# Performance work log

Hardware: AMD Instinct MI355X
Metric: run time of the kernel (lower is better)

The kernel has to match this reference:

```python
import jax, jax.numpy as jnp
import numpy as np

EPS = 1e-5
NUM_HEADS = 16
NUM_KV_HEADS = 4
NUM_EXPERTS = 8
TOP_K = 2


def _layernorm(x, w, b):
    mu = jnp.mean(x, axis=-1, keepdims=True)
    var = jnp.mean((x - mu) ** 2, axis=-1, keepdims=True)
    return (x - mu) * jax.lax.rsqrt(var + EPS) * w + b


def setup_inputs() -> dict:
    key = jax.random.key(0)
    ks = jax.random.split(key, 8)
    S, B, H = 1024, 4, 1024
    F = 2048
    hd = H // NUM_HEADS
    qkv_out = (NUM_HEADS + 2 * NUM_KV_HEADS) * hd  # 1536
    w_scale = 0.02
    return {
        "hidden_states": jax.random.normal(ks[0], (S, B, H), jnp.float32),
        "ln1_weight": jnp.ones((H,), jnp.float32),
        "ln1_bias": jnp.zeros((H,), jnp.float32),
        "ln2_weight": jnp.ones((H,), jnp.float32),
        "ln2_bias": jnp.zeros((H,), jnp.float32),
        "qkv_weight": jax.random.normal(ks[1], (qkv_out, H), jnp.float32) * w_scale,
        "proj_weight": jax.random.normal(ks[2], (H, H), jnp.float32) * w_scale,
        "router_weight": jax.random.normal(ks[3], (NUM_EXPERTS, H), jnp.float32) * w_scale,
        "moe_w1": jax.random.normal(ks[4], (NUM_EXPERTS, H, F), jnp.float32) * w_scale,
        "moe_w2": jax.random.normal(ks[5], (NUM_EXPERTS, F, H), jnp.float32) * w_scale,
    }


def reference(hidden_states, ln1_weight, ln1_bias, ln2_weight, ln2_bias,
              qkv_weight, proj_weight, router_weight, moe_w1, moe_w2):
    S, B, H = hidden_states.shape
    hd = H // NUM_HEADS
    rep = NUM_HEADS // NUM_KV_HEADS
    scale = 1.0 / hd ** 0.5

    # LN1 -> fused QKV projection
    ln1_out = _layernorm(hidden_states, ln1_weight, ln1_bias)
    qkv = jnp.einsum('sbh,oh->sbo', ln1_out, qkv_weight)
    q = qkv[..., :NUM_HEADS * hd].reshape(S, B, NUM_HEADS, hd)
    k = qkv[..., NUM_HEADS * hd:(NUM_HEADS + NUM_KV_HEADS) * hd].reshape(S, B, NUM_KV_HEADS, hd)
    v = qkv[..., (NUM_HEADS + NUM_KV_HEADS) * hd:].reshape(S, B, NUM_KV_HEADS, hd)

    # GQA: repeat KV heads to match query heads
    k = jnp.repeat(k, rep, axis=2)
    v = jnp.repeat(v, rep, axis=2)

    # causal scaled dot-product attention
    scores = jnp.einsum('sbhd,tbhd->bhst', q, k) * scale  # [B,h,S,S]
    causal = jnp.tril(jnp.ones((S, S), bool))
    scores = jnp.where(causal, scores, jnp.finfo(scores.dtype).min)
    probs = jax.nn.softmax(scores, axis=-1)
    attn = jnp.einsum('bhst,tbhd->sbhd', probs, v).reshape(S, B, H)

    proj_out = jnp.einsum('sbh,oh->sbo', attn, proj_weight)
    hidden_after_attn = hidden_states + proj_out

    # LN2 -> MoE
    ln2_out = _layernorm(hidden_after_attn, ln2_weight, ln2_bias)
    x = ln2_out.reshape(-1, H)  # [T,H]

    logits = jnp.einsum('th,eh->te', x, router_weight)
    gate = jax.nn.softmax(logits, axis=-1)
    top_probs, top_idx = jax.lax.top_k(gate, TOP_K)  # [T,K]

    # dense all-expert FFN (reference for grouped expert GEMMs)
    h_mid = jax.nn.gelu(jnp.einsum('th,ehf->etf', x, moe_w1))  # [E,T,F]
    expert_out = jnp.einsum('etf,efh->eth', h_mid, moe_w2)     # [E,T,H]

    # combine: weight[e,t] = sum_k top_probs[t,k] * (top_idx[t,k]==e)
    e_ids = jnp.arange(NUM_EXPERTS)[:, None, None]
    weights = jnp.sum(jnp.where(top_idx[None] == e_ids, top_probs[None], 0.0), axis=-1)  # [E,T]
    moe_out = jnp.einsum('eth,et->th', expert_out, weights).reshape(S, B, H)

    return hidden_after_attn + moe_out
```

## Files before the change

### kernel.cpp

```cpp
#include <hip/hip_runtime.h>
#include <stdint.h>

typedef unsigned short u16;
typedef float f32x4 __attribute__((ext_vector_type(4)));
typedef __bf16 bf16x8 __attribute__((ext_vector_type(8)));
typedef u16 u16x8 __attribute__((ext_vector_type(8)));

#define NHEADS 16
#define NKV 4
#define HD 64
#define HDIM 1024
#define FDIM 2048
#define SLEN 1024
#define BATCH 4
#define TTOK 4096
#define NEXP 8
#define QKVO 1536
#define K3 3072
#define NREP 32

__device__ __forceinline__ u16 f2bf(float f) {
  union { float f; uint32_t u; } c; c.f = f;
  uint32_t u = c.u;
  return (u16)((u + 0x7FFFu + ((u >> 16) & 1u)) >> 16);
}
__device__ __forceinline__ float bf2f(u16 h) {
  union { uint32_t u; float f; } c; c.u = ((uint32_t)h) << 16; return c.f;
}
__device__ __forceinline__ void split2(float v, u16& h, u16& l) {
  h = f2bf(v);
  l = f2bf(v - bf2f(h));
}

__device__ __forceinline__ f32x4 mfma16(bf16x8 a, bf16x8 b, f32x4 c) {
  return __builtin_amdgcn_mfma_f32_16x16x32_bf16(a, b, c, 0, 0, 0);
}

__device__ __forceinline__ bf16x8 lds_frag(const u16* base) {
  u16x8 v = *(const u16x8*)base;
  return __builtin_bit_cast(bf16x8, v);
}

__device__ __forceinline__ void gload_lds16(const void* g, void* l) {
  __builtin_amdgcn_global_load_lds((const __attribute__((address_space(1))) void*)g,
                                   (__attribute__((address_space(3))) void*)l, 16, 0, 0);
}

__global__ __launch_bounds__(256)
void cvt_w3_kernel(const float* __restrict__ in, u16* __restrict__ out, int n4) {
  int i = blockIdx.x * blockDim.x + threadIdx.x;
  if (i >= n4) return;
  float4 v = ((const float4*)in)[i];
  int row = i >> 8;
  int c = (i & 255) * 4;
  ushort4 h, l;
  split2(v.x, h.x, l.x); split2(v.y, h.y, l.y);
  split2(v.z, h.z, l.z); split2(v.w, h.w, l.w);
  u16* orow = out + (size_t)row * K3 + c;
  *(ushort4*)(orow) = h;
  *(ushort4*)(orow + 1024) = h;
  *(ushort4*)(orow + 2048) = l;
}

__global__ __launch_bounds__(256)
void transpose_cvt_kernel(const float* __restrict__ in, u16* __restrict__ out, int R, int C) {
  __shared__ float tile[32][33];
  size_t eoff = (size_t)blockIdx.z * (size_t)R * (size_t)C;
  in += eoff; out += eoff;
  int c0 = blockIdx.x * 32, r0 = blockIdx.y * 32;
  int tx = threadIdx.x, ty = threadIdx.y;
#pragma unroll
  for (int i = 0; i < 4; i++)
    tile[ty + i * 8][tx] = in[(size_t)(r0 + ty + i * 8) * C + c0 + tx];
  __syncthreads();
#pragma unroll
  for (int i = 0; i < 4; i++)
    out[(size_t)(c0 + ty + i * 8) * R + r0 + tx] = f2bf(tile[tx][ty + i * 8]);
}

__global__ __launch_bounds__(256)
void ln_kernel(const float* __restrict__ x, const float* __restrict__ w,
               const float* __restrict__ bias, u16* __restrict__ o3,
               u16* __restrict__ obf, float* __restrict__ of32) {
  int t = blockIdx.x, tid = threadIdx.x;
  int wid = tid >> 6, lane = tid & 63;
  float4 v = ((const float4*)(x + (size_t)t * HDIM))[tid];
  float s = v.x + v.y + v.z + v.w;
  float q = v.x * v.x + v.y * v.y + v.z * v.z + v.w * v.w;
#pragma unroll
  for (int mm = 32; mm >= 1; mm >>= 1) {
    s += __shfl_xor(s, mm);
    q += __shfl_xor(q, mm);
  }
  __shared__ float ss[4], qq[4];
  if (lane == 0) { ss[wid] = s; qq[wid] = q; }
  __syncthreads();
  s = ss[0] + ss[1] + ss[2] + ss[3];
  q = qq[0] + qq[1] + qq[2] + qq[3];
  float mu = s * (1.0f / HDIM);
  float var = q * (1.0f / HDIM) - mu * mu;
  float inv = rsqrtf(var + 1e-5f);
  float4 wv = ((const float4*)w)[tid];
  float4 bv = ((const float4*)bias)[tid];
  float y0 = (v.x - mu) * inv * wv.x + bv.x;
  float y1 = (v.y - mu) * inv * wv.y + bv.y;
  float y2 = (v.z - mu) * inv * wv.z + bv.z;
  float y3 = (v.w - mu) * inv * wv.w + bv.w;
  ushort4 h, l;
  split2(y0, h.x, l.x); split2(y1, h.y, l.y);
  split2(y2, h.z, l.z); split2(y3, h.w, l.w);
  if (o3) {
    u16* orow = o3 + (size_t)t * K3 + tid * 4;
    *(ushort4*)(orow) = h;
    *(ushort4*)(orow + 1024) = l;
    *(ushort4*)(orow + 2048) = h;
  }
  if (obf) ((ushort4*)(obf + (size_t)t * HDIM))[tid] = h;
  if (of32) {
    float4 yo; yo.x = y0; yo.y = y1; yo.z = y2; yo.w = y3;
    ((float4*)(of32 + (size_t)t * HDIM))[tid] = yo;
  }
}

template<int MODE>
__global__ __launch_bounds__(256)
void gemm_bt(const u16* __restrict__ A0, const u16* __restrict__ B0,
             int N, int K, int M,
             const float* __restrict__ resid, float* __restrict__ outf,
             u16* __restrict__ o0, u16* __restrict__ o1, u16* __restrict__ o2,
             u16* __restrict__ o3, u16* __restrict__ o4, u16* __restrict__ o5,
             const int* __restrict__ offs, const int* __restrict__ rowsIdx,
             const float* __restrict__ wts) {
  int tid = threadIdx.x;
  int wid = tid >> 6, lane = tid & 63;
  int l15 = lane & 15, l4 = lane >> 4;
  int bn = blockIdx.x, bm = blockIdx.y, e = blockIdx.z;

  int Me = M, rowBase = 0;
  const u16* A = A0;
  const u16* B = B0;
  if constexpr (MODE == 2 || MODE == 3) {
    int oa = offs[e], ob = offs[e + 1];
    Me = ob - oa; rowBase = oa;
    B = B0 + (size_t)e * (size_t)N * (size_t)K;
    if constexpr (MODE == 3) A = A0 + (size_t)oa * (size_t)K;
  }
  if (bm * 128 >= Me) return;

  __shared__ u16 lsA[2][128 * 64];
  __shared__ u16 lsB[2][128 * 64];

  int slot = tid & 7;
  const u16* aPtr[4];
  const u16* bPtr[4];
#pragma unroll
  for (int i = 0; i < 4; i++) {
    int r = i * 32 + (tid >> 3);
    int sl = slot ^ (r & 7);
    int rg = bm * 128 + r;
    if constexpr (MODE == 2) {
      int rc = rg < Me ? rg : (Me - 1);
      rg = rowsIdx[rowBase + rc];
    } else if constexpr (MODE == 3) {
      rg = rg < Me ? rg : (Me - 1);
    }
    aPtr[i] = A + (size_t)rg * K + sl * 8;
    int ng = bn * 128 + r;
    bPtr[i] = B + (size_t)ng * K + sl * 8;
  }

  int wm = (wid >> 1) * 64, wn = (wid & 1) * 64;
  f32x4 zero4 = {0.f, 0.f, 0.f, 0.f};
  f32x4 acc[4][4];
#pragma unroll
  for (int mi = 0; mi < 4; mi++)
#pragma unroll
    for (int ni = 0; ni < 4; ni++) acc[mi][ni] = zero4;

  int aoff[4][2], boff[4][2];
#pragma unroll
  for (int mi = 0; mi < 4; mi++) {
    int row = wm + mi * 16 + l15;
#pragma unroll
    for (int kk = 0; kk < 2; kk++) {
      int cs = kk * 4 + l4;
      aoff[mi][kk] = row * 64 + ((cs ^ (row & 7)) << 3);
    }
  }
#pragma unroll
  for (int ni = 0; ni < 4; ni++) {
    int row = wn + ni * 16 + l15;
#pragma unroll
    for (int kk = 0; kk < 2; kk++) {
      int cs = kk * 4 + l4;
      boff[ni][kk] = row * 64 + ((cs ^ (row & 7)) << 3);
    }
  }

  int nk = K >> 6;
#pragma unroll
  for (int i = 0; i < 4; i++) {
    gload_lds16(aPtr[i], &lsA[0][(i * 256 + wid * 64) * 8]);
    gload_lds16(bPtr[i], &lsB[0][(i * 256 + wid * 64) * 8]);
  }
  __syncthreads();

  int buf = 0;
  for (int kt = 0; kt < nk; ++kt) {
    if (kt + 1 < nk) {
      int k0 = (kt + 1) << 6;
#pragma unroll
      for (int i = 0; i < 4; i++) {
        gload_lds16(aPtr[i] + k0, &lsA[buf ^ 1][(i * 256 + wid * 64) * 8]);
        gload_lds16(bPtr[i] + k0, &lsB[buf ^ 1][(i * 256 + wid * 64) * 8]);
      }
    }
#pragma unroll
    for (int kk = 0; kk < 2; kk++) {
      bf16x8 af[4], bfr[4];
#pragma unroll
      for (int mi = 0; mi < 4; mi++) af[mi] = lds_frag(&lsA[buf][aoff[mi][kk]]);
#pragma unroll
      for (int ni = 0; ni < 4; ni++) bfr[ni] = lds_frag(&lsB[buf][boff[ni][kk]]);
#pragma unroll
      for (int mi = 0; mi < 4; mi++)
#pragma unroll
        for (int ni = 0; ni < 4; ni++)
          acc[mi][ni] = mfma16(af[mi], bfr[ni], acc[mi][ni]);
    }
    __syncthreads();
    buf ^= 1;
  }

#pragma unroll
  for (int mi = 0; mi < 4; mi++) {
#pragma unroll
    for (int r = 0; r < 4; r++) {
      int m = bm * 128 + wm + mi * 16 + l4 * 4 + r;
      if (m >= Me) continue;
#pragma unroll
      for (int ni = 0; ni < 4; ni++) {
        int n = bn * 128 + wn + ni * 16 + l15;
        float v = acc[mi][ni][r];
        if constexpr (MODE == 0) {
          u16 hh, ll; split2(v, hh, ll);
          int sq = m >> 2, bb = m & 3;
          int d = n & 63;
          if (n < 1024) {
            int hd = n >> 6;
            size_t o = ((size_t)(bb * NHEADS + hd) * SLEN + sq) * HD + d;
            o0[o] = hh; o1[o] = ll;
          } else if (n < 1280) {
            int hd = (n - 1024) >> 6;
            size_t o = ((size_t)(bb * NKV + hd) * SLEN + sq) * HD + d;
            o2[o] = hh; o3[o] = ll;
          } else {
            int hd = (n - 1280) >> 6;
            size_t o = ((size_t)(bb * NKV + hd) * SLEN + sq) * HD + d;
            o4[o] = hh; o5[o] = ll;
          }
        } else if constexpr (MODE == 1) {
          size_t idx = (size_t)m * HDIM + n;
          outf[idx] = v + resid[idx];
        } else if constexpr (MODE == 2) {
          float g = 0.5f * v * (1.0f + tanhf(0.7978845608f * (v + 0.044715f * v * v * v)));
          o0[(size_t)(rowBase + m) * FDIM + n] = f2bf(g);
        } else {
          outf[(size_t)(rowBase + m) * HDIM + n] = v * wts[rowBase + m];
        }
      }
    }
  }
}

__global__ __launch_bounds__(256)
void attn_kernel(const u16* __restrict__ Qh_, const u16* __restrict__ Ql_,
                 const u16* __restrict__ Kh_, const u16* __restrict__ Kl_,
                 const u16* __restrict__ Vh_, const u16* __restrict__ Vl_,
                 u16* __restrict__ A3) {
  int bh = blockIdx.x;
  int qt = blockIdx.y;
  int b = bh >> 4, h = bh & 15, kh = h >> 2;
  int tid = threadIdx.x, wid = tid >> 6, lane = tid & 63;
  int l15 = lane & 15, l4 = lane >> 4;
  int slot = tid & 7;

  size_t qoff = ((size_t)(b * NHEADS + h) * SLEN) * HD;
  size_t koff = ((size_t)(b * NKV + kh) * SLEN) * HD;
  const u16* Qh = Qh_ + qoff;
  const u16* Ql = Ql_ + qoff;
  const u16* Kh = Kh_ + koff;
  const u16* Kl = Kl_ + koff;
  const u16* Vh = Vh_ + koff;
  const u16* Vl = Vl_ + koff;

  __shared__ u16 KtH[2][4096], KtL[2][4096];
  __shared__ u16 VtH[4096], VtL[4096];
  __shared__ u16 PtH[4][1024], PtL[4][1024];

  int qrow = qt * 64 + wid * 16 + l15;
  bf16x8 qfh[2], qfl[2];
#pragma unroll
  for (int kk = 0; kk < 2; kk++) {
    u16x8 vh = *(const u16x8*)(Qh + (size_t)qrow * HD + kk * 32 + l4 * 8);
    u16x8 vl = *(const u16x8*)(Ql + (size_t)qrow * HD + kk * 32 + l4 * 8);
    qfh[kk] = __builtin_bit_cast(bf16x8, vh);
    qfl[kk] = __builtin_bit_cast(bf16x8, vl);
  }

  int kr0 = tid >> 3;
  int kr1 = 32 + (tid >> 3);
  int sl0 = slot ^ (kr0 & 7);
  int sl1 = slot ^ (kr1 & 7);
  int kdst0 = (0 * 256 + wid * 64) * 8;
  int kdst1 = (1 * 256 + wid * 64) * 8;

#define STAGE_K(kt_, bf_)                                                     \
  {                                                                           \
    size_t s0 = (size_t)((kt_)*64 + kr0) * HD + sl0 * 8;                      \
    size_t s1 = (size_t)((kt_)*64 + kr1) * HD + sl1 * 8;                      \
    gload_lds16(Kh + s0, &KtH[bf_][kdst0]);                                   \
    gload_lds16(Kl + s0, &KtL[bf_][kdst0]);                                   \
    gload_lds16(Kh + s1, &KtH[bf_][kdst1]);                                   \
    gload_lds16(Kl + s1, &KtL[bf_][kdst1]);                                   \
  }

#define LOAD_V(kt_, vh_, vl_)                                                 \
  {                                                                           \
    _Pragma("unroll") for (int i = 0; i < 2; i++) {                           \
      int kv = i * 32 + (tid >> 3);                                           \
      (vh_)[i] = *(const uint4*)(Vh + (size_t)((kt_)*64 + kv) * HD + slot * 8);\
      (vl_)[i] = *(const uint4*)(Vl + (size_t)((kt_)*64 + kv) * HD + slot * 8);\
    }                                                                         \
  }

#define SCATTER_V(vh_, vl_)                                                   \
  {                                                                           \
    _Pragma("unroll") for (int i = 0; i < 2; i++) {                           \
      int kv = i * 32 + (tid >> 3);                                           \
      const u16* ph = (const u16*)&(vh_)[i];                                  \
      const u16* pl = (const u16*)&(vl_)[i];                                  \
      _Pragma("unroll") for (int j = 0; j < 8; j++) {                         \
        int d = slot * 8 + j;                                                 \
        int g = ((kv >> 3) ^ (d & 7) ^ (d >> 3)) & 7;                         \
        int addr = d * 64 + (g << 3) + (kv & 7);                              \
        VtH[addr] = ph[j];                                                    \
        VtL[addr] = pl[j];                                                    \
      }                                                                       \
    }                                                                         \
  }

  uint4 vH[2], vL[2];
  STAGE_K(0, 0);
  LOAD_V(0, vH, vL);
  SCATTER_V(vH, vL);
  __syncthreads();

  f32x4 zero4 = {0.f, 0.f, 0.f, 0.f};
  f32x4 oacc[4];
#pragma unroll
  for (int nf = 0; nf < 4; nf++) oacc[nf] = zero4;
  float mrun[4], lrun[4];
#pragma unroll
  for (int r = 0; r < 4; r++) { mrun[r] = -1e30f; lrun[r] = 0.f; }

  int buf = 0;
  for (int kt = 0; kt <= qt; ++kt) {
    int kv0 = kt * 64;
    if (kt < qt) {
      STAGE_K(kt + 1, buf ^ 1);
      LOAD_V(kt + 1, vH, vL);
    }

    f32x4 sacc[4];
#pragma unroll
    for (int nf = 0; nf < 4; nf++) sacc[nf] = zero4;
#pragma unroll
    for (int kk = 0; kk < 2; kk++) {
#pragma unroll
      for (int nf = 0; nf < 4; nf++) {
        int krow = nf * 16 + l15;
        int ka = krow * 64 + (((kk * 4 + l4) ^ (krow & 7)) << 3);
        bf16x8 kfh = lds_frag(&KtH[buf][ka]);
        bf16x8 kfl = lds_frag(&KtL[buf][ka]);
        sacc[nf] = mfma16(qfh[kk], kfh, sacc[nf]);
        sacc[nf] = mfma16(qfh[kk], kfl, sacc[nf]);
        sacc[nf] = mfma16(qfl[kk], kfh, sacc[nf]);
      }
    }

    bool diag = (kt == qt);
    float tm[4];
#pragma unroll
    for (int r = 0; r < 4; r++) tm[r] = -1e30f;
#pragma unroll
    for (int nf = 0; nf < 4; nf++) {
#pragma unroll
      for (int r = 0; r < 4; r++) {
        float s = sacc[nf][r] * 0.125f;
        if (diag) {
          int qg = qt * 64 + wid * 16 + l4 * 4 + r;
          int kg = kv0 + nf * 16 + l15;
          if (kg > qg) s = -1e30f;
        }
        sacc[nf][r] = s;
        tm[r] = fmaxf(tm[r], s);
      }
    }
#pragma unroll
    for (int mm = 1; mm < 16; mm <<= 1) {
#pragma unroll
      for (int r = 0; r < 4; r++) tm[r] = fmaxf(tm[r], __shfl_xor(tm[r], mm));
    }
    float ts[4];
#pragma unroll
    for (int r = 0; r < 4; r++) {
      float mn = fmaxf(mrun[r], tm[r]);
      float al = __expf(mrun[r] - mn);
      mrun[r] = mn;
      lrun[r] *= al;
#pragma unroll
      for (int nf = 0; nf < 4; nf++) oacc[nf][r] *= al;
      ts[r] = 0.f;
    }
#pragma unroll
    for (int nf = 0; nf < 4; nf++) {
#pragma unroll
      for (int r = 0; r < 4; r++) {
        float p = __expf(sacc[nf][r] - mrun[r]);
        sacc[nf][r] = p;
        ts[r] += p;
      }
    }
#pragma unroll
    for (int mm = 1; mm < 16; mm <<= 1) {
#pragma unroll
      for (int r = 0; r < 4; r++) ts[r] += __shfl_xor(ts[r], mm);
    }
#pragma unroll
    for (int r = 0; r < 4; r++) lrun[r] += ts[r];

#pragma unroll
    for (int nf = 0; nf < 4; nf++) {
#pragma unroll
      for (int r = 0; r < 4; r++) {
        int qrl = l4 * 4 + r;
        int kv = nf * 16 + l15;
        int g = ((kv >> 3) ^ (qrl & 7) ^ (qrl >> 3)) & 7;
        int addr = qrl * 64 + (g << 3) + (kv & 7);
        u16 hh, ll;
        split2(sacc[nf][r], hh, ll);
        PtH[wid][addr] = hh;
        PtL[wid][addr] = ll;
      }
    }
#pragma unroll
    for (int s2 = 0; s2 < 2; s2++) {
      int cs = s2 * 4 + l4;
      int pa = l15 * 64 + ((((cs ^ (l15 & 7) ^ (l15 >> 3))) & 7) << 3);
      bf16x8 pfh = lds_frag(&PtH[wid][pa]);
      bf16x8 pfl = lds_frag(&PtL[wid][pa]);
#pragma unroll
      for (int nf = 0; nf < 4; nf++) {
        int d = nf * 16 + l15;
        int va = d * 64 + ((((cs ^ (d & 7) ^ (d >> 3))) & 7) << 3);
        bf16x8 vfh = lds_frag(&VtH[va]);
        bf16x8 vfl = lds_frag(&VtL[va]);
        oacc[nf] = mfma16(pfh, vfh, oacc[nf]);
        oacc[nf] = mfma16(pfh, vfl, oacc[nf]);
        oacc[nf] = mfma16(pfl, vfh, oacc[nf]);
      }
    }

    __syncthreads();
    if (kt < qt) {
      SCATTER_V(vH, vL);
    }
    __syncthreads();
    buf ^= 1;
  }

#pragma unroll
  for (int r = 0; r < 4; r++) {
    float invl = 1.0f / lrun[r];
    int qg = qt * 64 + wid * 16 + l4 * 4 + r;
    size_t tb = ((size_t)qg * BATCH + b) * K3 + h * HD;
#pragma unroll
    for (int nf = 0; nf < 4; nf++) {
      u16 hh, ll;
      split2(oacc[nf][r] * invl, hh, ll);
      size_t o = tb + nf * 16 + l15;
      A3[o] = hh;
      A3[o + 1024] = ll;
      A3[o + 2048] = hh;
    }
  }
#undef STAGE_K
#undef LOAD_V
#undef SCATTER_V
}

__global__ __launch_bounds__(256)
void router_kernel(const float* __restrict__ x, const float* __restrict__ rw,
                   int* __restrict__ tidx, float* __restrict__ tp) {
  int t = blockIdx.x, tid = threadIdx.x;
  int wid = tid >> 6, lane = tid & 63;
  float4 xv = ((const float4*)(x + (size_t)t * HDIM))[tid];
  __shared__ float part[8][4];
  __shared__ float lg[8];
#pragma unroll
  for (int e = 0; e < 8; e++) {
    float4 wv = ((const float4*)(rw + (size_t)e * HDIM))[tid];
    float d = xv.x * wv.x + xv.y * wv.y + xv.z * wv.z + xv.w * wv.w;
#pragma unroll
    for (int mm = 32; mm >= 1; mm >>= 1) d += __shfl_xor(d, mm);
    if (lane == 0) part[e][wid] = d;
  }
  __syncthreads();
  if (tid < 8) lg[tid] = part[tid][0] + part[tid][1] + part[tid][2] + part[tid][3];
  __syncthreads();
  if (tid == 0) {
    float mx = lg[0];
#pragma unroll
    for (int e = 1; e < 8; e++) mx = fmaxf(mx, lg[e]);
    float g[8]; float se = 0.f;
#pragma unroll
    for (int e = 0; e < 8; e++) { g[e] = __expf(lg[e] - mx); se += g[e]; }
    float inv = 1.0f / se;
#pragma unroll
    for (int e = 0; e < 8; e++) g[e] *= inv;
    int i0 = 0; float v0 = g[0];
#pragma unroll
    for (int e = 1; e < 8; e++) if (g[e] > v0) { v0 = g[e]; i0 = e; }
    int i1 = -1; float v1 = -1.f;
#pragma unroll
    for (int e = 0; e < 8; e++) if (e != i0 && g[e] > v1) { v1 = g[e]; i1 = e; }
    tidx[t * 2] = i0; tidx[t * 2 + 1] = i1;
    tp[t * 2] = v0; tp[t * 2 + 1] = v1;
  }
}

__global__ __launch_bounds__(256)
void hist_offsets_kernel(const int* __restrict__ tidx, int* __restrict__ offs,
                         int* __restrict__ repBase, int* __restrict__ curRep) {
  __shared__ int hist[NEXP * NREP];
  __shared__ int eoffs[NEXP + 1];
  int tid = threadIdx.x;
  hist[tid] = 0;
  __syncthreads();
  for (int i = tid; i < TTOK; i += 256) {
    int rep = i & (NREP - 1);
    atomicAdd(&hist[tidx[2 * i] * NREP + rep], 1);
    atomicAdd(&hist[tidx[2 * i + 1] * NREP + rep], 1);
  }
  __syncthreads();
  if (tid == 0) {
    int a = 0;
    for (int e = 0; e < NEXP; e++) {
      eoffs[e] = a;
      for (int r = 0; r < NREP; r++) a += hist[e * NREP + r];
    }
    eoffs[NEXP] = a;
  }
  __syncthreads();
  if (tid < NEXP) {
    int a = eoffs[tid];
    for (int r = 0; r < NREP; r++) {
      repBase[tid * NREP + r] = a;
      a += hist[tid * NREP + r];
    }
  }
  if (tid < NEXP + 1) offs[tid] = eoffs[tid];
  curRep[tid] = 0;
}

__global__ __launch_bounds__(256)
void assign_kernel(const int* __restrict__ tidx, const float* __restrict__ tp,
                   const int* __restrict__ repBase, int* __restrict__ curRep,
                   int* __restrict__ rowsIdx, float* __restrict__ wvals,
                   int* __restrict__ inv) {
  int t = blockIdx.x * blockDim.x + threadIdx.x;
  if (t >= TTOK) return;
  int rep = t & (NREP - 1);
#pragma unroll
  for (int k = 0; k < 2; k++) {
    int e = tidx[t * 2 + k];
    int s = atomicAdd(&curRep[e * NREP + rep], 1);
    int pos = repBase[e * NREP + rep] + s;
    rowsIdx[pos] = t;
    wvals[pos] = tp[t * 2 + k];
    inv[t * 2 + k] = pos;
  }
}

__global__ __launch_bounds__(256)
void combine_kernel(float* __restrict__ out, const float* __restrict__ eo,
                    const int* __restrict__ inv) {
  int t = blockIdx.x, c = threadIdx.x;
  int r0 = inv[t * 2], r1 = inv[t * 2 + 1];
  float4* o = (float4*)(out + (size_t)t * HDIM);
  const float4* e0 = (const float4*)(eo + (size_t)r0 * HDIM);
  const float4* e1 = (const float4*)(eo + (size_t)r1 * HDIM);
  float4 v = o[c];
  float4 a = e0[c];
  float4 bb = e1[c];
  v.x += a.x + bb.x; v.y += a.y + bb.y; v.z += a.z + bb.z; v.w += a.w + bb.w;
  o[c] = v;
}

extern "C" void kernel_launch(void* const* d_in, const int* in_sizes, int n_in,
                              void* d_out, int out_size, void* d_ws, size_t ws_size,
                              hipStream_t stream) {
  (void)in_sizes; (void)n_in; (void)out_size; (void)ws_size;
  const float* hs    = (const float*)d_in[0];
  const float* ln1w  = (const float*)d_in[1];
  const float* ln1b  = (const float*)d_in[2];
  const float* ln2w  = (const float*)d_in[3];
  const float* ln2b  = (const float*)d_in[4];
  const float* wqkv  = (const float*)d_in[5];
  const float* wproj = (const float*)d_in[6];
  const float* wrout = (const float*)d_in[7];
  const float* w1    = (const float*)d_in[8];
  const float* w2    = (const float*)d_in[9];
  float* out = (float*)d_out;

  char* base = (char*)d_ws;
  size_t off = 0;
  auto alloc = [&](size_t n) { void* r = base + off; off += (n + 255) & ~(size_t)255; return r; };

  const size_t SZ_W1T   = (size_t)NEXP * FDIM * HDIM * 2;
  const size_t SZ_W2T   = (size_t)NEXP * HDIM * FDIM * 2;
  const size_t SZ_WP3   = (size_t)HDIM * K3 * 2;
  const size_t SZ_LN13  = (size_t)TTOK * K3 * 2;
  const size_t SZ_WQ3   = (size_t)QKVO * K3 * 2;
  const size_t SZ_HMID  = (size_t)TTOK * 2 * FDIM * 2;
  const size_t SZ_Q     = (size_t)BATCH * NHEADS * SLEN * HD * 2;
  const size_t SZ_KV    = (size_t)BATCH * NKV * SLEN * HD * 2;
  const size_t SZ_A3    = (size_t)TTOK * K3 * 2;
  const size_t SZ_EO    = (size_t)TTOK * 2 * HDIM * 4;

  u16* w1t     = (u16*)alloc(SZ_W1T);
  u16* w2t     = (u16*)alloc(SZ_W2T);
  u16* wproj3  = (u16*)alloc(SZ_WP3);

  size_t r1sz = SZ_LN13 + SZ_WQ3;
  if (SZ_HMID > r1sz) r1sz = SZ_HMID;
  char* r1 = (char*)alloc(r1sz);
  u16* ln1_3 = (u16*)r1;
  u16* wqkv3 = (u16*)(r1 + SZ_LN13);
  u16* hmid  = (u16*)r1;

  size_t r2sz = 2 * SZ_Q + 4 * SZ_KV + SZ_A3;
  if (SZ_EO > r2sz) r2sz = SZ_EO;
  char* r2 = (char*)alloc(r2sz);
  u16* Qbh = (u16*)r2;
  u16* Qbl = (u16*)(r2 + SZ_Q);
  u16* Kbh = (u16*)(r2 + 2 * SZ_Q);
  u16* Kbl = (u16*)(r2 + 2 * SZ_Q + SZ_KV);
  u16* Vbh = (u16*)(r2 + 2 * SZ_Q + 2 * SZ_KV);
  u16* Vbl = (u16*)(r2 + 2 * SZ_Q + 3 * SZ_KV);
  u16* attn3 = (u16*)(r2 + 2 * SZ_Q + 4 * SZ_KV);
  float* eo = (float*)r2;

  u16* ln2o    = (u16*)alloc((size_t)TTOK * HDIM * 2);
  float* ln2f  = (float*)alloc((size_t)TTOK * HDIM * 4);
  int* tidx    = (int*)alloc(TTOK * 2 * 4);
  float* tp    = (float*)alloc(TTOK * 2 * 4);
  int* rowsIdx = (int*)alloc(TTOK * 2 * 4);
  float* wvals = (float*)alloc(TTOK * 2 * 4);
  int* invm    = (int*)alloc(TTOK * 2 * 4);
  int* offs    = (int*)alloc((NEXP + 1) * 4);
  int* repBase = (int*)alloc(NEXP * NREP * 4);
  int* curRep  = (int*)alloc(NEXP * NREP * 4);

  cvt_w3_kernel<<<(QKVO * HDIM / 4 + 255) / 256, 256, 0, stream>>>(wqkv, wqkv3, QKVO * HDIM / 4);
  cvt_w3_kernel<<<(HDIM * HDIM / 4 + 255) / 256, 256, 0, stream>>>(wproj, wproj3, HDIM * HDIM / 4);
  dim3 tb(32, 8);
  transpose_cvt_kernel<<<dim3(FDIM / 32, HDIM / 32, NEXP), tb, 0, stream>>>(w1, w1t, HDIM, FDIM);
  transpose_cvt_kernel<<<dim3(HDIM / 32, FDIM / 32, NEXP), tb, 0, stream>>>(w2, w2t, FDIM, HDIM);

  ln_kernel<<<TTOK, 256, 0, stream>>>(hs, ln1w, ln1b, ln1_3, nullptr, nullptr);

  gemm_bt<0><<<dim3(QKVO / 128, TTOK / 128), 256, 0, stream>>>(
      ln1_3, wqkv3, QKVO, K3, TTOK, nullptr, nullptr,
      Qbh, Qbl, Kbh, Kbl, Vbh, Vbl, nullptr, nullptr, nullptr);

  attn_kernel<<<dim3(BATCH * NHEADS, SLEN / 64), 256, 0, stream>>>(
      Qbh, Qbl, Kbh, Kbl, Vbh, Vbl, attn3);

  gemm_bt<1><<<dim3(HDIM / 128, TTOK / 128), 256, 0, stream>>>(
      attn3, wproj3, HDIM, K3, TTOK, hs, out,
      nullptr, nullptr, nullptr, nullptr, nullptr, nullptr, nullptr, nullptr, nullptr);

  ln_kernel<<<TTOK, 256, 0, stream>>>(out, ln2w, ln2b, nullptr, ln2o, ln2f);

  router_kernel<<<TTOK, 256, 0, stream>>>(ln2f, wrout, tidx, tp);
  hist_offsets_kernel<<<1, 256, 0, stream>>>(tidx, offs, repBase, curRep);
  assign_kernel<<<TTOK / 256, 256, 0, stream>>>(tidx, tp, repBase, curRep, rowsIdx, wvals, invm);

  gemm_bt<2><<<dim3(FDIM / 128, TTOK / 128, NEXP), 256, 0, stream>>>(
      ln2o, w1t, FDIM, HDIM, 0, nullptr, nullptr,
      hmid, nullptr, nullptr, nullptr, nullptr, nullptr, offs, rowsIdx, nullptr);

  gemm_bt<3><<<dim3(HDIM / 128, TTOK / 128, NEXP), 256, 0, stream>>>(
      hmid, w2t, HDIM, FDIM, 0, nullptr, eo,
      nullptr, nullptr, nullptr, nullptr, nullptr, nullptr, offs, nullptr, wvals);

  combine_kernel<<<TTOK, 256, 0, stream>>>(out, eo, invm);
}
```

Baseline: 484.5 us.

## Shrink split-bf16 operands to 2K layout, add XCD remap and larger MoE tiles

```diff
diff --git a/kernel.cpp b/kernel.cpp
--- a/kernel.cpp
+++ b/kernel.cpp
@@ -16,7 +16,7 @@
 #define TTOK 4096
 #define NEXP 8
 #define QKVO 1536
-#define K3 3072
+#define K2 2048
 #define NREP 32
 
 __device__ __forceinline__ u16 f2bf(float f) {
@@ -47,7 +47,7 @@
 }
 
 __global__ __launch_bounds__(256)
-void cvt_w3_kernel(const float* __restrict__ in, u16* __restrict__ out, int n4) {
+void cvt_w2_kernel(const float* __restrict__ in, u16* __restrict__ out, int n4) {
   int i = blockIdx.x * blockDim.x + threadIdx.x;
   if (i >= n4) return;
   float4 v = ((const float4*)in)[i];
@@ -56,10 +56,9 @@
   ushort4 h, l;
   split2(v.x, h.x, l.x); split2(v.y, h.y, l.y);
   split2(v.z, h.z, l.z); split2(v.w, h.w, l.w);
-  u16* orow = out + (size_t)row * K3 + c;
+  u16* orow = out + (size_t)row * K2 + c;
   *(ushort4*)(orow) = h;
-  *(ushort4*)(orow + 1024) = h;
-  *(ushort4*)(orow + 2048) = l;
+  *(ushort4*)(orow + 1024) = l;
 }
 
 __global__ __launch_bounds__(256)
@@ -80,7 +79,7 @@
 
 __global__ __launch_bounds__(256)
 void ln_kernel(const float* __restrict__ x, const float* __restrict__ w,
-               const float* __restrict__ bias, u16* __restrict__ o3,
+               const float* __restrict__ bias, u16* __restrict__ o2,
                u16* __restrict__ obf, float* __restrict__ of32) {
   int t = blockIdx.x, tid = threadIdx.x;
   int wid = tid >> 6, lane = tid & 63;
@@ -109,11 +108,10 @@
   ushort4 h, l;
   split2(y0, h.x, l.x); split2(y1, h.y, l.y);
   split2(y2, h.z, l.z); split2(y3, h.w, l.w);
-  if (o3) {
-    u16* orow = o3 + (size_t)t * K3 + tid * 4;
+  if (o2) {
+    u16* orow = o2 + (size_t)t * K2 + tid * 4;
     *(ushort4*)(orow) = h;
     *(ushort4*)(orow + 1024) = l;
-    *(ushort4*)(orow + 2048) = h;
   }
   if (obf) ((ushort4*)(obf + (size_t)t * HDIM))[tid] = h;
   if (of32) {
@@ -122,19 +120,31 @@
   }
 }
 
-template<int MODE>
-__global__ __launch_bounds__(256)
+template<int MODE, int TB, int BM>
+__global__ __launch_bounds__(TB, 2)
 void gemm_bt(const u16* __restrict__ A0, const u16* __restrict__ B0,
-             int N, int K, int M,
+             int kstride, int nk, int M,
              const float* __restrict__ resid, float* __restrict__ outf,
              u16* __restrict__ o0, u16* __restrict__ o1, u16* __restrict__ o2,
              u16* __restrict__ o3, u16* __restrict__ o4, u16* __restrict__ o5,
              const int* __restrict__ offs, const int* __restrict__ rowsIdx,
              const float* __restrict__ wts) {
+  constexpr int BN = 128;
+  constexpr int IA = BM / (TB / 8);
+  constexpr int IB = BN / (TB / 8);
   int tid = threadIdx.x;
   int wid = tid >> 6, lane = tid & 63;
   int l15 = lane & 15, l4 = lane >> 4;
-  int bn = blockIdx.x, bm = blockIdx.y, e = blockIdx.z;
+  int slot = tid & 7;
+
+  int gx = gridDim.x;
+  int nwg = gx * gridDim.y;
+  int flat = blockIdx.y * gx + blockIdx.x;
+  int q8 = nwg >> 3, r8 = nwg & 7;
+  int xcd = flat & 7, idx = flat >> 3;
+  int nf = (xcd < r8 ? xcd * (q8 + 1) : r8 * (q8 + 1) + (xcd - r8) * q8) + idx;
+  int bn = nf % gx, bm = nf / gx;
+  int e = blockIdx.z;
 
   int Me = M, rowBase = 0;
   const u16* A = A0;
@@ -142,31 +152,34 @@
   if constexpr (MODE == 2 || MODE == 3) {
     int oa = offs[e], ob = offs[e + 1];
     Me = ob - oa; rowBase = oa;
-    B = B0 + (size_t)e * (size_t)N * (size_t)K;
-    if constexpr (MODE == 3) A = A0 + (size_t)oa * (size_t)K;
-  }
-  if (bm * 128 >= Me) return;
-
-  __shared__ u16 lsA[2][128 * 64];
-  __shared__ u16 lsB[2][128 * 64];
-
-  int slot = tid & 7;
-  const u16* aPtr[4];
-  const u16* bPtr[4];
-#pragma unroll
-  for (int i = 0; i < 4; i++) {
-    int r = i * 32 + (tid >> 3);
+    B = B0 + (size_t)e * (size_t)(MODE == 2 ? FDIM : HDIM) * (size_t)kstride;
+    if constexpr (MODE == 3) A = A0 + (size_t)oa * (size_t)kstride;
+  }
+  if (bm * BM >= Me) return;
+
+  __shared__ u16 lsA[2][BM * 64];
+  __shared__ u16 lsB[2][BN * 64];
+
+  const u16* aPtr[IA];
+  const u16* bPtr[IB];
+#pragma unroll
+  for (int i = 0; i < IA; i++) {
+    int r = (i * TB + tid) >> 3;
     int sl = slot ^ (r & 7);
-    int rg = bm * 128 + r;
+    int rg = bm * BM + r;
     if constexpr (MODE == 2) {
       int rc = rg < Me ? rg : (Me - 1);
       rg = rowsIdx[rowBase + rc];
     } else if constexpr (MODE == 3) {
       rg = rg < Me ? rg : (Me - 1);
     }
-    aPtr[i] = A + (size_t)rg * K + sl * 8;
-    int ng = bn * 128 + r;
-    bPtr[i] = B + (size_t)ng * K + sl * 8;
+    aPtr[i] = A + (size_t)rg * kstride + sl * 8;
+  }
+#pragma unroll
+  for (int i = 0; i < IB; i++) {
+    int r = (i * TB + tid) >> 3;
+    int sl = slot ^ (r & 7);
+    bPtr[i] = B + (size_t)(bn * BN + r) * kstride + sl * 8;
   }
 
   int wm = (wid >> 1) * 64, wn = (wid & 1) * 64;
@@ -197,23 +210,33 @@
     }
   }
 
-  int nk = K >> 6;
-#pragma unroll
-  for (int i = 0; i < 4; i++) {
-    gload_lds16(aPtr[i], &lsA[0][(i * 256 + wid * 64) * 8]);
-    gload_lds16(bPtr[i], &lsB[0][(i * 256 + wid * 64) * 8]);
-  }
+  auto ksched = [&](int kt, int& ak, int& bk) {
+    if constexpr (MODE <= 1) {
+      int ph = kt >> 4, kl = kt & 15;
+      ak = (ph == 1 ? 1024 : 0) + kl * 64;
+      bk = (ph == 2 ? 1024 : 0) + kl * 64;
+    } else {
+      ak = kt << 6;
+      bk = ak;
+    }
+  };
+
+  int ak, bk;
+  ksched(0, ak, bk);
+#pragma unroll
+  for (int i = 0; i < IA; i++) gload_lds16(aPtr[i] + ak, &lsA[0][(i * TB + wid * 64) * 8]);
+#pragma unroll
+  for (int i = 0; i < IB; i++) gload_lds16(bPtr[i] + bk, &lsB[0][(i * TB + wid * 64) * 8]);
   __syncthreads();
 
   int buf = 0;
   for (int kt = 0; kt < nk; ++kt) {
     if (kt + 1 < nk) {
-      int k0 = (kt + 1) << 6;
-#pragma unroll
-      for (int i = 0; i < 4; i++) {
-        gload_lds16(aPtr[i] + k0, &lsA[buf ^ 1][(i * 256 + wid * 64) * 8]);
-        gload_lds16(bPtr[i] + k0, &lsB[buf ^ 1][(i * 256 + wid * 64) * 8]);
-      }
+      ksched(kt + 1, ak, bk);
+#pragma unroll
+      for (int i = 0; i < IA; i++) gload_lds16(aPtr[i] + ak, &lsA[buf ^ 1][(i * TB + wid * 64) * 8]);
+#pragma unroll
+      for (int i = 0; i < IB; i++) gload_lds16(bPtr[i] + bk, &lsB[buf ^ 1][(i * TB + wid * 64) * 8]);
     }
 #pragma unroll
     for (int kk = 0; kk < 2; kk++) {
@@ -236,11 +259,11 @@
   for (int mi = 0; mi < 4; mi++) {
 #pragma unroll
     for (int r = 0; r < 4; r++) {
-      int m = bm * 128 + wm + mi * 16 + l4 * 4 + r;
+      int m = bm * BM + wm + mi * 16 + l4 * 4 + r;
       if (m >= Me) continue;
 #pragma unroll
       for (int ni = 0; ni < 4; ni++) {
-        int n = bn * 128 + wn + ni * 16 + l15;
+        int n = bn * BN + wn + ni * 16 + l15;
         float v = acc[mi][ni][r];
         if constexpr (MODE == 0) {
           u16 hh, ll; split2(v, hh, ll);
@@ -260,8 +283,8 @@
             o4[o] = hh; o5[o] = ll;
           }
         } else if constexpr (MODE == 1) {
-          size_t idx = (size_t)m * HDIM + n;
-          outf[idx] = v + resid[idx];
+          size_t iidx = (size_t)m * HDIM + n;
+          outf[iidx] = v + resid[iidx];
         } else if constexpr (MODE == 2) {
           float g = 0.5f * v * (1.0f + tanhf(0.7978845608f * (v + 0.044715f * v * v * v)));
           o0[(size_t)(rowBase + m) * FDIM + n] = f2bf(g);
@@ -277,7 +300,7 @@
 void attn_kernel(const u16* __restrict__ Qh_, const u16* __restrict__ Ql_,
                  const u16* __restrict__ Kh_, const u16* __restrict__ Kl_,
                  const u16* __restrict__ Vh_, const u16* __restrict__ Vl_,
-                 u16* __restrict__ A3) {
+                 u16* __restrict__ A2) {
   int bh = blockIdx.x;
   int qt = blockIdx.y;
   int b = bh >> 4, h = bh & 15, kh = h >> 2;
@@ -484,15 +507,14 @@
   for (int r = 0; r < 4; r++) {
     float invl = 1.0f / lrun[r];
     int qg = qt * 64 + wid * 16 + l4 * 4 + r;
-    size_t tb = ((size_t)qg * BATCH + b) * K3 + h * HD;
+    size_t tb = ((size_t)qg * BATCH + b) * K2 + h * HD;
 #pragma unroll
     for (int nf = 0; nf < 4; nf++) {
       u16 hh, ll;
       split2(oacc[nf][r] * invl, hh, ll);
       size_t o = tb + nf * 16 + l15;
-      A3[o] = hh;
-      A3[o + 1024] = ll;
-      A3[o + 2048] = hh;
+      A2[o] = hh;
+      A2[o + 1024] = ll;
     }
   }
 #undef STAGE_K
@@ -630,27 +652,27 @@
 
   const size_t SZ_W1T   = (size_t)NEXP * FDIM * HDIM * 2;
   const size_t SZ_W2T   = (size_t)NEXP * HDIM * FDIM * 2;
-  const size_t SZ_WP3   = (size_t)HDIM * K3 * 2;
-  const size_t SZ_LN13  = (size_t)TTOK * K3 * 2;
-  const size_t SZ_WQ3   = (size_t)QKVO * K3 * 2;
+  const size_t SZ_WP2   = (size_t)HDIM * K2 * 2;
+  const size_t SZ_LN12  = (size_t)TTOK * K2 * 2;
+  const size_t SZ_WQ2   = (size_t)QKVO * K2 * 2;
   const size_t SZ_HMID  = (size_t)TTOK * 2 * FDIM * 2;
   const size_t SZ_Q     = (size_t)BATCH * NHEADS * SLEN * HD * 2;
   const size_t SZ_KV    = (size_t)BATCH * NKV * SLEN * HD * 2;
-  const size_t SZ_A3    = (size_t)TTOK * K3 * 2;
+  const size_t SZ_A2    = (size_t)TTOK * K2 * 2;
   const size_t SZ_EO    = (size_t)TTOK * 2 * HDIM * 4;
 
   u16* w1t     = (u16*)alloc(SZ_W1T);
   u16* w2t     = (u16*)alloc(SZ_W2T);
-  u16* wproj3  = (u16*)alloc(SZ_WP3);
-
-  size_t r1sz = SZ_LN13 + SZ_WQ3;
+  u16* wproj2  = (u16*)alloc(SZ_WP2);
+
+  size_t r1sz = SZ_LN12 + SZ_WQ2;
   if (SZ_HMID > r1sz) r1sz = SZ_HMID;
   char* r1 = (char*)alloc(r1sz);
-  u16* ln1_3 = (u16*)r1;
-  u16* wqkv3 = (u16*)(r1 + SZ_LN13);
+  u16* ln1_2 = (u16*)r1;
+  u16* wqkv2 = (u16*)(r1 + SZ_LN12);
   u16* hmid  = (u16*)r1;
 
-  size_t r2sz = 2 * SZ_Q + 4 * SZ_KV + SZ_A3;
+  size_t r2sz = 2 * SZ_Q + 4 * SZ_KV + SZ_A2;
   if (SZ_EO > r2sz) r2sz = SZ_EO;
   char* r2 = (char*)alloc(r2sz);
   u16* Qbh = (u16*)r2;
@@ -659,7 +681,7 @@
   u16* Kbl = (u16*)(r2 + 2 * SZ_Q + SZ_KV);
   u16* Vbh = (u16*)(r2 + 2 * SZ_Q + 2 * SZ_KV);
   u16* Vbl = (u16*)(r2 + 2 * SZ_Q + 3 * SZ_KV);
-  u16* attn3 = (u16*)(r2 + 2 * SZ_Q + 4 * SZ_KV);
+  u16* attn2 = (u16*)(r2 + 2 * SZ_Q + 4 * SZ_KV);
   float* eo = (float*)r2;
 
   u16* ln2o    = (u16*)alloc((size_t)TTOK * HDIM * 2);
@@ -673,23 +695,23 @@
   int* repBase = (int*)alloc(NEXP * NREP * 4);
   int* curRep  = (int*)alloc(NEXP * NREP * 4);
 
-  cvt_w3_kernel<<<(QKVO * HDIM / 4 + 255) / 256, 256, 0, stream>>>(wqkv, wqkv3, QKVO * HDIM / 4);
-  cvt_w3_kernel<<<(HDIM * HDIM / 4 + 255) / 256, 256, 0, stream>>>(wproj, wproj3, HDIM * HDIM / 4);
+  cvt_w2_kernel<<<(QKVO * HDIM / 4 + 255) / 256, 256, 0, stream>>>(wqkv, wqkv2, QKVO * HDIM / 4);
+  cvt_w2_kernel<<<(HDIM * HDIM / 4 + 255) / 256, 256, 0, stream>>>(wproj, wproj2, HDIM * HDIM / 4);
   dim3 tb(32, 8);
   transpose_cvt_kernel<<<dim3(FDIM / 32, HDIM / 32, NEXP), tb, 0, stream>>>(w1, w1t, HDIM, FDIM);
   transpose_cvt_kernel<<<dim3(HDIM / 32, FDIM / 32, NEXP), tb, 0, stream>>>(w2, w2t, FDIM, HDIM);
 
-  ln_kernel<<<TTOK, 256, 0, stream>>>(hs, ln1w, ln1b, ln1_3, nullptr, nullptr);
-
-  gemm_bt<0><<<dim3(QKVO / 128, TTOK / 128), 256, 0, stream>>>(
-      ln1_3, wqkv3, QKVO, K3, TTOK, nullptr, nullptr,
+  ln_kernel<<<TTOK, 256, 0, stream>>>(hs, ln1w, ln1b, ln1_2, nullptr, nullptr);
+
+  gemm_bt<0, 256, 128><<<dim3(QKVO / 128, TTOK / 128), 256, 0, stream>>>(
+      ln1_2, wqkv2, K2, 48, TTOK, nullptr, nullptr,
       Qbh, Qbl, Kbh, Kbl, Vbh, Vbl, nullptr, nullptr, nullptr);
 
   attn_kernel<<<dim3(BATCH * NHEADS, SLEN / 64), 256, 0, stream>>>(
-      Qbh, Qbl, Kbh, Kbl, Vbh, Vbl, attn3);
-
-  gemm_bt<1><<<dim3(HDIM / 128, TTOK / 128), 256, 0, stream>>>(
-      attn3, wproj3, HDIM, K3, TTOK, hs, out,
+      Qbh, Qbl, Kbh, Kbl, Vbh, Vbl, attn2);
+
+  gemm_bt<1, 256, 128><<<dim3(HDIM / 128, TTOK / 128), 256, 0, stream>>>(
+      attn2, wproj2, K2, 48, TTOK, hs, out,
       nullptr, nullptr, nullptr, nullptr, nullptr, nullptr, nullptr, nullptr, nullptr);
 
   ln_kernel<<<TTOK, 256, 0, stream>>>(out, ln2w, ln2b, nullptr, ln2o, ln2f);
@@ -698,12 +720,12 @@
   hist_offsets_kernel<<<1, 256, 0, stream>>>(tidx, offs, repBase, curRep);
   assign_kernel<<<TTOK / 256, 256, 0, stream>>>(tidx, tp, repBase, curRep, rowsIdx, wvals, invm);
 
-  gemm_bt<2><<<dim3(FDIM / 128, TTOK / 128, NEXP), 256, 0, stream>>>(
-      ln2o, w1t, FDIM, HDIM, 0, nullptr, nullptr,
+  gemm_bt<2, 512, 256><<<dim3(FDIM / 128, 16, NEXP), 512, 0, stream>>>(
+      ln2o, w1t, HDIM, 16, 0, nullptr, nullptr,
       hmid, nullptr, nullptr, nullptr, nullptr, nullptr, offs, rowsIdx, nullptr);
 
-  gemm_bt<3><<<dim3(HDIM / 128, TTOK / 128, NEXP), 256, 0, stream>>>(
-      hmid, w2t, HDIM, FDIM, 0, nullptr, eo,
+  gemm_bt<3, 512, 256><<<dim3(HDIM / 128, 16, NEXP), 512, 0, stream>>>(
+      hmid, w2t, FDIM, 32, 0, nullptr, eo,
       nullptr, nullptr, nullptr, nullptr, nullptr, nullptr, offs, nullptr, wvals);
 
   combine_kernel<<<TTOK, 256, 0, stream>>>(out, eo, invm);
```

New measurement: 701.8 us. 1.45x slower.
